# Performance work log

Hardware: AMD Instinct MI355X
Metric: run time of the kernel (lower is better)

## Reference

```python
import jax, jax.numpy as jnp
import numpy as np

E, M, K, N = 32, 1024, 512, 512

def setup_inputs() -> dict:
    key = jax.random.key(0)
    k1, k2, k3 = jax.random.split(key, 3)
    A = jax.random.normal(k1, (E, M, K), dtype=jnp.float32)
    B = jax.random.normal(k2, (E, N, K), dtype=jnp.float32)
    expert_num_tokens = jax.random.randint(k3, (E,), 0, M + 1, dtype=jnp.int32)
    return {"A": A, "B": B, "expert_num_tokens": expert_num_tokens}

def reference(A, B, expert_num_tokens):
    # Per-expert GEMM: C[e] = A[e] @ B[e].T  -> [E, M, N]
    C = jnp.einsum('emk,enk->emn', A, B)
    # Rows m >= expert_num_tokens[e] are never computed/stored by the kernel;
    # zero them in the reference output.
    row_valid = jnp.arange(A.shape[1])[None, :] < expert_num_tokens[:, None]  # [E, M]
    return jnp.where(row_valid[:, :, None], C, jnp.zeros((), C.dtype))
```

## Files before the change

### kernel.cpp

```cpp
#include <hip/hip_runtime.h>
#include <hip/hip_bf16.h>

#define NE 32
#define MM 1024
#define KK 512
#define NN 512
#define BM 128
#define BN 128
#define BK 32

typedef __attribute__((ext_vector_type(8))) short bf16x8;
typedef __attribute__((ext_vector_type(4))) float floatx4;

__device__ __forceinline__ short f2bf(float f) {
  union { __hip_bfloat16 b; short s; } u;
  u.b = __float2bfloat16(f);
  return u.s;
}

extern "C" __global__ __launch_bounds__(256, 4)
void expert_gemm(const float* __restrict__ A, const float* __restrict__ B,
                 const int* __restrict__ cnts, float* __restrict__ C)
{
  const int b   = blockIdx.x;
  const int tid = threadIdx.x;

  int e = -1, mt = 0, nt = 0;
  int acc = 0;
#pragma unroll 1
  for (int i = 0; i < NE; ++i) {
    int vt = (cnts[i] + BM - 1) >> 7;
    int c4 = vt << 2;
    if (e < 0 && b < acc + c4) { int r = b - acc; e = i; mt = r >> 2; nt = r & 3; }
    acc += c4;
  }
  if (e < 0) {
    int z = b - acc, a2 = 0;
#pragma unroll 1
    for (int i = 0; i < NE; ++i) {
      int vt = (cnts[i] + BM - 1) >> 7;
      int c = 8 - vt;
      if (e < 0 && z < a2 + c) { e = i; mt = vt + (z - a2); }
      a2 += c;
    }
    if (e < 0) return;
    float* Ce = C + ((size_t)e * MM + mt * BM) * NN;
    float4 zf = make_float4(0.f, 0.f, 0.f, 0.f);
#pragma unroll
    for (int i = 0; i < 64; ++i) {
      int fidx = i * 256 + tid;
      int r = fidx >> 7, c = (fidx & 127) << 2;
      *(float4*)(Ce + (size_t)r * NN + c) = zf;
    }
    return;
  }

  const int m0 = mt * BM, n0 = nt * BN;
  const int cnt = cnts[e];
  const float* Ae = A + ((size_t)e * MM + m0) * KK;
  const float* Be = B + ((size_t)e * NN + n0) * KK;
  float* Ce = C + ((size_t)e * MM + m0) * NN + n0;

  __shared__ __align__(16) short lA[BM * BK];
  __shared__ __align__(16) short lB[BN * BK];

  const int wave = tid >> 6, lane = tid & 63;
  const int wm = (wave >> 1) * 64, wn = (wave & 1) * 64;
  const int fr = lane & 15, kh = lane >> 4;

  const int srow = tid >> 2;
  const int su   = tid & 3;

  floatx4 acc4[4][4] = {};

  for (int kt = 0; kt < KK; kt += BK) {
    float4 a0[2], a1[2], b0[2], b1[2];
#pragma unroll
    for (int p = 0; p < 2; ++p) {
      int row = srow + (p << 6);
      int col = kt + (su << 3);
      a0[p] = *(const float4*)(Ae + (size_t)row * KK + col);
      a1[p] = *(const float4*)(Ae + (size_t)row * KK + col + 4);
      b0[p] = *(const float4*)(Be + (size_t)row * KK + col);
      b1[p] = *(const float4*)(Be + (size_t)row * KK + col + 4);
    }

    __syncthreads();
#pragma unroll
    for (int p = 0; p < 2; ++p) {
      int row = srow + (p << 6);
      int unit = (row << 2) + (su ^ (row & 3));
      bf16x8 va = { f2bf(a0[p].x), f2bf(a0[p].y), f2bf(a0[p].z), f2bf(a0[p].w),
                    f2bf(a1[p].x), f2bf(a1[p].y), f2bf(a1[p].z), f2bf(a1[p].w) };
      bf16x8 vb = { f2bf(b0[p].x), f2bf(b0[p].y), f2bf(b0[p].z), f2bf(b0[p].w),
                    f2bf(b1[p].x), f2bf(b1[p].y), f2bf(b1[p].z), f2bf(b1[p].w) };
      *(bf16x8*)(lA + (unit << 3)) = va;
      *(bf16x8*)(lB + (unit << 3)) = vb;
    }
    __syncthreads();

    bf16x8 af[4], bfv[4];
#pragma unroll
    for (int i = 0; i < 4; ++i) {
      int rA = wm + (i << 4) + fr;
      af[i]  = *(const bf16x8*)(lA + ((((rA << 2) + (kh ^ (rA & 3)))) << 3));
      int rB = wn + (i << 4) + fr;
      bfv[i] = *(const bf16x8*)(lB + ((((rB << 2) + (kh ^ (rB & 3)))) << 3));
    }
#pragma unroll
    for (int i = 0; i < 4; ++i)
#pragma unroll
      for (int j = 0; j < 4; ++j)
        acc4[i][j] = __builtin_amdgcn_mfma_f32_16x16x32_bf16(af[i], bfv[j], acc4[i][j], 0, 0, 0);
  }

  const int rb_ = (lane >> 4) * 4;
#pragma unroll
  for (int i = 0; i < 4; ++i) {
#pragma unroll
    for (int r = 0; r < 4; ++r) {
      int row = wm + i * 16 + rb_ + r;
      bool valid = (m0 + row) < cnt;
#pragma unroll
      for (int j = 0; j < 4; ++j) {
        int col = wn + j * 16 + fr;
        Ce[(size_t)row * NN + col] = valid ? acc4[i][j][r] : 0.0f;
      }
    }
  }
}

extern "C" void kernel_launch(void* const* d_in, const int* in_sizes, int n_in,
                              void* d_out, int out_size, void* d_ws, size_t ws_size,
                              hipStream_t stream) {
  const float* A    = (const float*)d_in[0];
  const float* B    = (const float*)d_in[1];
  const int*   cnts = (const int*)d_in[2];
  float*       C    = (float*)d_out;

  hipLaunchKernelGGL(expert_gemm, dim3(1024), dim3(256), 0, stream, A, B, cnts, C);
}
```

Measured before the change: 158.8 us.

## Halve M tile to 64 and register-prefetch next K slice

Shrinks the block tile from 128x128 to 64x128 and doubles the grid, so the valid-token rounding is finer and fewer padded rows get computed. It also adds register double-buffering: global loads for the next K step are issued before the current step converts to bf16, writes LDS and runs MFMA, hiding load latency. In exchange, B is re-read from global memory twice as often per output, and the prefetch buffers add register pressure, hence the lower launch-bounds occupancy hint.

After: 158.4 us. No clear change (-0.3%).

```diff
diff --git a/kernel.cpp b/kernel.cpp
--- a/kernel.cpp
+++ b/kernel.cpp
@@ -5,7 +5,7 @@
 #define MM 1024
 #define KK 512
 #define NN 512
-#define BM 128
+#define BM 64
 #define BN 128
 #define BK 32
 
@@ -18,7 +18,7 @@
   return u.s;
 }
 
-extern "C" __global__ __launch_bounds__(256, 4)
+extern "C" __global__ __launch_bounds__(256, 3)
 void expert_gemm(const float* __restrict__ A, const float* __restrict__ B,
                  const int* __restrict__ cnts, float* __restrict__ C)
 {
@@ -29,7 +29,7 @@
   int acc = 0;
 #pragma unroll 1
   for (int i = 0; i < NE; ++i) {
-    int vt = (cnts[i] + BM - 1) >> 7;
+    int vt = (cnts[i] + BM - 1) >> 6;
     int c4 = vt << 2;
     if (e < 0 && b < acc + c4) { int r = b - acc; e = i; mt = r >> 2; nt = r & 3; }
     acc += c4;
@@ -38,8 +38,8 @@
     int z = b - acc, a2 = 0;
 #pragma unroll 1
     for (int i = 0; i < NE; ++i) {
-      int vt = (cnts[i] + BM - 1) >> 7;
-      int c = 8 - vt;
+      int vt = (cnts[i] + BM - 1) >> 6;
+      int c = 16 - vt;
       if (e < 0 && z < a2 + c) { e = i; mt = vt + (z - a2); }
       a2 += c;
     }
@@ -47,7 +47,7 @@
     float* Ce = C + ((size_t)e * MM + mt * BM) * NN;
     float4 zf = make_float4(0.f, 0.f, 0.f, 0.f);
 #pragma unroll
-    for (int i = 0; i < 64; ++i) {
+    for (int i = 0; i < 32; ++i) {
       int fidx = i * 256 + tid;
       int r = fidx >> 7, c = (fidx & 127) << 2;
       *(float4*)(Ce + (size_t)r * NN + c) = zf;
@@ -65,61 +65,80 @@
   __shared__ __align__(16) short lB[BN * BK];
 
   const int wave = tid >> 6, lane = tid & 63;
-  const int wm = (wave >> 1) * 64, wn = (wave & 1) * 64;
+  const int wm = (wave >> 1) * 32, wn = (wave & 1) * 64;
   const int fr = lane & 15, kh = lane >> 4;
 
-  const int srow = tid >> 2;
-  const int su   = tid & 3;
+  const int sr = tid >> 2;
+  const int su = tid & 3;
 
-  floatx4 acc4[4][4] = {};
+  floatx4 acc4[2][4] = {};
 
+  float4 ra[2], rbv[4], na[2], nb[4];
+
+#define ISSUE(pa, pb, kt_) do {                                          \
+    int col_ = (kt_) + (su << 3);                                        \
+    pa[0] = *(const float4*)(Ae + (size_t)sr * KK + col_);               \
+    pa[1] = *(const float4*)(Ae + (size_t)sr * KK + col_ + 4);           \
+    pb[0] = *(const float4*)(Be + (size_t)sr * KK + col_);               \
+    pb[1] = *(const float4*)(Be + (size_t)sr * KK + col_ + 4);           \
+    pb[2] = *(const float4*)(Be + (size_t)(sr + 64) * KK + col_);        \
+    pb[3] = *(const float4*)(Be + (size_t)(sr + 64) * KK + col_ + 4);    \
+  } while (0)
+
+  ISSUE(ra, rbv, 0);
+
+#pragma unroll
   for (int kt = 0; kt < KK; kt += BK) {
-    float4 a0[2], a1[2], b0[2], b1[2];
-#pragma unroll
-    for (int p = 0; p < 2; ++p) {
-      int row = srow + (p << 6);
-      int col = kt + (su << 3);
-      a0[p] = *(const float4*)(Ae + (size_t)row * KK + col);
-      a1[p] = *(const float4*)(Ae + (size_t)row * KK + col + 4);
-      b0[p] = *(const float4*)(Be + (size_t)row * KK + col);
-      b1[p] = *(const float4*)(Be + (size_t)row * KK + col + 4);
-    }
+    if (kt + BK < KK) ISSUE(na, nb, kt + BK);
+
+    bf16x8 va  = { f2bf(ra[0].x),  f2bf(ra[0].y),  f2bf(ra[0].z),  f2bf(ra[0].w),
+                   f2bf(ra[1].x),  f2bf(ra[1].y),  f2bf(ra[1].z),  f2bf(ra[1].w) };
+    bf16x8 vb0 = { f2bf(rbv[0].x), f2bf(rbv[0].y), f2bf(rbv[0].z), f2bf(rbv[0].w),
+                   f2bf(rbv[1].x), f2bf(rbv[1].y), f2bf(rbv[1].z), f2bf(rbv[1].w) };
+    bf16x8 vb1 = { f2bf(rbv[2].x), f2bf(rbv[2].y), f2bf(rbv[2].z), f2bf(rbv[2].w),
+                   f2bf(rbv[3].x), f2bf(rbv[3].y), f2bf(rbv[3].z), f2bf(rbv[3].w) };
 
     __syncthreads();
-#pragma unroll
-    for (int p = 0; p < 2; ++p) {
-      int row = srow + (p << 6);
-      int unit = (row << 2) + (su ^ (row & 3));
-      bf16x8 va = { f2bf(a0[p].x), f2bf(a0[p].y), f2bf(a0[p].z), f2bf(a0[p].w),
-                    f2bf(a1[p].x), f2bf(a1[p].y), f2bf(a1[p].z), f2bf(a1[p].w) };
-      bf16x8 vb = { f2bf(b0[p].x), f2bf(b0[p].y), f2bf(b0[p].z), f2bf(b0[p].w),
-                    f2bf(b1[p].x), f2bf(b1[p].y), f2bf(b1[p].z), f2bf(b1[p].w) };
-      *(bf16x8*)(lA + (unit << 3)) = va;
-      *(bf16x8*)(lB + (unit << 3)) = vb;
+    {
+      int u0 = (sr << 2) + (su ^ (sr & 3));
+      *(bf16x8*)(lA + (u0 << 3)) = va;
+      *(bf16x8*)(lB + (u0 << 3)) = vb0;
+      int r1 = sr + 64;
+      int u1 = (r1 << 2) + (su ^ (r1 & 3));
+      *(bf16x8*)(lB + (u1 << 3)) = vb1;
     }
     __syncthreads();
 
-    bf16x8 af[4], bfv[4];
+    bf16x8 af[2], bfv[4];
 #pragma unroll
-    for (int i = 0; i < 4; ++i) {
+    for (int i = 0; i < 2; ++i) {
       int rA = wm + (i << 4) + fr;
       af[i]  = *(const bf16x8*)(lA + ((((rA << 2) + (kh ^ (rA & 3)))) << 3));
-      int rB = wn + (i << 4) + fr;
-      bfv[i] = *(const bf16x8*)(lB + ((((rB << 2) + (kh ^ (rB & 3)))) << 3));
     }
 #pragma unroll
-    for (int i = 0; i < 4; ++i)
+    for (int j = 0; j < 4; ++j) {
+      int rB = wn + (j << 4) + fr;
+      bfv[j] = *(const bf16x8*)(lB + ((((rB << 2) + (kh ^ (rB & 3)))) << 3));
+    }
+#pragma unroll
+    for (int i = 0; i < 2; ++i)
 #pragma unroll
       for (int j = 0; j < 4; ++j)
         acc4[i][j] = __builtin_amdgcn_mfma_f32_16x16x32_bf16(af[i], bfv[j], acc4[i][j], 0, 0, 0);
+
+#pragma unroll
+    for (int q = 0; q < 2; ++q) ra[q] = na[q];
+#pragma unroll
+    for (int q = 0; q < 4; ++q) rbv[q] = nb[q];
   }
+#undef ISSUE
 
-  const int rb_ = (lane >> 4) * 4;
+  const int rbase = (lane >> 4) * 4;
 #pragma unroll
-  for (int i = 0; i < 4; ++i) {
+  for (int i = 0; i < 2; ++i) {
 #pragma unroll
     for (int r = 0; r < 4; ++r) {
-      int row = wm + i * 16 + rb_ + r;
+      int row = wm + i * 16 + rbase + r;
       bool valid = (m0 + row) < cnt;
 #pragma unroll
       for (int j = 0; j < 4; ++j) {
@@ -138,5 +157,5 @@
   const int*   cnts = (const int*)d_in[2];
   float*       C    = (float*)d_out;
 
-  hipLaunchKernelGGL(expert_gemm, dim3(1024), dim3(256), 0, stream, A, B, cnts, C);
+  hipLaunchKernelGGL(expert_gemm, dim3(2048), dim3(256), 0, stream, A, B, cnts, C);
 }
```
